# Optimization experiments

Hardware: AMD Instinct MI355X
Metric: run time of the kernel (lower is better)

Reference implementation:

```python
import jax, jax.numpy as jnp
import numpy as np

E, IN, OUT, GS, N = 8, 1024, 2816, 64, 2048
G = IN // GS  # 16 quantization groups along in_features


def setup_inputs() -> dict:
    key = jax.random.key(0)
    k0, k1, k2, k3 = jax.random.split(key, 4)
    x = jax.random.normal(k0, (N, IN), dtype=jnp.float32)
    # tokens are contiguous per expert; counts must sum exactly to N
    cuts = np.sort(np.random.default_rng(0).integers(0, N + 1, size=E - 1))
    counts = np.diff(np.concatenate([[0], cuts, [N]]))
    tokens_per_expert = jnp.asarray(counts, dtype=jnp.int32)
    # int4 codes stored as int32 in [0, 16)
    W_q = jax.random.randint(k1, (E, IN, OUT), 0, 16, dtype=jnp.int32)
    scales = jax.random.uniform(k2, (E, G, OUT), dtype=jnp.float32, minval=1e-3, maxval=2e-2)
    zeros = jax.random.uniform(k3, (E, G, OUT), dtype=jnp.float32, minval=0.0, maxval=15.0)
    return {"input": x, "tokens_per_expert": tokens_per_expert,
            "W_q": W_q, "scales": scales, "zeros": zeros}


def _dequant(W_q, scales, zeros):
    # HQQ-style asymmetric dequant: W = (W_q - zero) * scale, per group of GS
    # rows along in_features.  W_q: [E, IN, OUT] -> [E, G, GS, OUT]
    e, in_f, out_f = W_q.shape
    g = scales.shape[1]
    gs = in_f // g
    Wf = W_q.astype(scales.dtype).reshape(e, g, gs, out_f)
    W = (Wf - zeros[:, :, None, :]) * scales[:, :, None, :]
    return W.reshape(e, in_f, out_f)


def reference(input, tokens_per_expert, W_q, scales, zeros):
    # Dequantize all expert weights: [E, IN, OUT]
    W = _dequant(W_q, scales, zeros)
    # Expert id per token from exclusive-cumsum boundaries (tokens are sorted
    # by expert, contiguous slices [cumsum[e], cumsum[e+1]) ).
    boundaries = jnp.cumsum(tokens_per_expert)  # [E]
    tok = jnp.arange(input.shape[0])
    seg = jnp.searchsorted(boundaries, tok, side='right')  # [N] expert per token
    # Grouped GEMM expressed densely (jit-safe): compute x @ W_e for all e,
    # then select each token's own expert output.
    y_all = jnp.einsum('nd,edo->neo', input, W)  # [N, E, OUT]
    y = jnp.take_along_axis(y_all, seg[:, None, None], axis=1)[:, 0, :]
    return y
```

## Files before the change

### kernel.cpp

```cpp
#include <hip/hip_runtime.h>
#include <hip/hip_bf16.h>
#include <stdint.h>


namespace {
constexpr int kE = 8;
constexpr int kIn = 1024;
constexpr int kOut = 2816;
constexpr int kGroups = 16;
constexpr int kTok = 2048;
constexpr int kXStride = kIn + 64;
constexpr int kBM = 64;
constexpr int kBN = 128;
constexpr int kBTS = 72;
constexpr int kNT = kOut / kBN;
constexpr int kGrid = kNT * 256;
}

typedef __attribute__((ext_vector_type(8))) short short8;
typedef __attribute__((ext_vector_type(4))) float f32x4;
typedef __attribute__((ext_vector_type(4))) int i32x4;
typedef __attribute__((ext_vector_type(4))) unsigned int u32x4;

static __device__ __forceinline__ uint32_t fbits(float f) {
  union { float f; uint32_t u; } v; v.f = f; return v.u;
}
static __device__ __forceinline__ unsigned short bf16_rne(float f) {
  uint32_t u = fbits(f);
  u += 0x7fffu + ((u >> 16) & 1u);
  return (unsigned short)(u >> 16);
}
static __device__ __forceinline__ float bf16_f(unsigned short h) {
  union { uint32_t u; float f; } v; v.u = ((uint32_t)h) << 16; return v.f;
}

__global__ __launch_bounds__(256) void hqq_prep(const float* __restrict__ x,
                                                unsigned short* __restrict__ xhi,
                                                unsigned short* __restrict__ xlo) {
  const int row = blockIdx.x;
  const int tid = threadIdx.x;
  const f32x4 v = *(const f32x4*)(x + (size_t)row * kIn + tid * 4);
  unsigned long long hp = 0, lp = 0;
  float s = 0.f;
#pragma unroll
  for (int j = 0; j < 4; ++j) {
    float f = v[j];
    unsigned short h = bf16_rne(f);
    unsigned short l = bf16_rne(f - bf16_f(h));
    hp |= ((unsigned long long)h) << (16 * j);
    lp |= ((unsigned long long)l) << (16 * j);
    s += f;
  }
  *(unsigned long long*)(xhi + (size_t)row * kXStride + tid * 4) = hp;
  *(unsigned long long*)(xlo + (size_t)row * kXStride + tid * 4) = lp;
#pragma unroll
  for (int m = 1; m <= 8; m <<= 1) s += __shfl_xor(s, m, 64);
  if ((tid & 15) == 0) {
    const int g = tid >> 4;
    unsigned short rhi = bf16_rne(s);
    unsigned short rlo = bf16_rne(s - bf16_f(rhi));
    unsigned short* p = xhi + (size_t)row * kXStride + kIn;
    p[g] = rhi; p[16 + g] = rhi; p[32 + g] = rlo; p[48 + g] = 0;
    unsigned short* q = xlo + (size_t)row * kXStride + kIn;
    q[g] = 0; q[16 + g] = 0; q[32 + g] = 0; q[48 + g] = 0;
  }
}

__global__ __launch_bounds__(256, 2) void hqq_gemm(
    const unsigned short* __restrict__ xhi, const unsigned short* __restrict__ xlo,
    const int* __restrict__ wq, const float* __restrict__ scales,
    const float* __restrict__ zeros, const int* __restrict__ tpe,
    float* __restrict__ out) {
  __shared__ unsigned short Bt[2][kBN * kBTS];

  const int raw = blockIdx.x;
  const int bid = (raw & 7) * (kGrid / 8) + (raw >> 3);

  const int nt = bid >> 8;
  const int em = bid & 255;
  const int e = em >> 5;
  const int mt = em & 31;

  int e_start = 0, cnt = 0, cum = 0;
#pragma unroll
  for (int i = 0; i < kE; ++i) {
    int c = tpe[i];
    if (i == e) { e_start = cum; cnt = c; }
    cum += c;
  }
  if (mt * kBM >= cnt) return;
  const int e_end = e_start + cnt;
  const int row0 = e_start + mt * kBM;
  const int nn = nt * kBN;

  const int tid = threadIdx.x;
  const int lane = tid & 63;
  const int wid = tid >> 6;
  const int wm = wid >> 1;
  const int wn = wid & 1;

  size_t arow[2];
#pragma unroll
  for (int mf = 0; mf < 2; ++mf) {
    int r = row0 + wm * 32 + mf * 16 + (lane & 15);
    if (r > kTok - 1) r = kTok - 1;
    arow[mf] = (size_t)r * kXStride;
  }

  const int oq = tid & 31;
  const int kc = tid >> 5;
  const int* wbase = wq + (size_t)e * kIn * kOut + (size_t)(kc * 8) * kOut + nn + oq * 4;
  const int btw_off = (oq * 4) * kBTS + kc * 8;

  const float* sc_base = scales + (size_t)e * kGroups * kOut + nn + wn * 64 + (lane & 15);

  i32x4 w[8];
  auto loadB = [&](int g) {
    const int* p = wbase + (size_t)g * 64 * kOut;
#pragma unroll
    for (int i = 0; i < 8; ++i) w[i] = *(const i32x4*)(p + (size_t)i * kOut);
  };
  auto writeB = [&](int buf) {
    unsigned short* btw = &Bt[buf][btw_off];
#pragma unroll
    for (int j = 0; j < 4; ++j) {
      u32x4 o;
#pragma unroll
      for (int ww = 0; ww < 4; ++ww) {
        uint32_t b0 = fbits((float)w[2 * ww][j]);
        uint32_t b1 = fbits((float)w[2 * ww + 1][j]);
        o[ww] = (b0 >> 16) | (b1 & 0xffff0000u);
      }
      *(u32x4*)(btw + j * kBTS) = o;
    }
  };

  f32x4 acc[2][4];
#pragma unroll
  for (int a = 0; a < 2; ++a)
#pragma unroll
    for (int b = 0; b < 4; ++b) acc[a][b] = 0.f;

  loadB(0);
  writeB(0);
  __syncthreads();

  for (int g = 0; g <= 16; ++g) {
    if (g < 15) loadB(g + 1);

    float sc[4];
#pragma unroll
    for (int nf = 0; nf < 4; ++nf)
      sc[nf] = (g < kGroups) ? sc_base[(size_t)g * kOut + nf * 16] : 1.f;

    f32x4 S[2][4];
#pragma unroll
    for (int a = 0; a < 2; ++a)
#pragma unroll
      for (int b = 0; b < 4; ++b) S[a][b] = 0.f;

    const unsigned short* btb = &Bt[g & 1][0];
#pragma unroll
    for (int ks = 0; ks < 2; ++ks) {
      const int k0l = ks * 32 + (lane >> 4) * 8;
      const int k0g = g * 64 + k0l;
      short8 ah[2], al[2], bb[4];
#pragma unroll
      for (int mf = 0; mf < 2; ++mf) {
        ah[mf] = *(const short8*)&xhi[arow[mf] + k0g];
        al[mf] = *(const short8*)&xlo[arow[mf] + k0g];
      }
#pragma unroll
      for (int nf = 0; nf < 4; ++nf) {
        const int nrow = wn * 64 + nf * 16 + (lane & 15);
        bb[nf] = *(const short8*)&btb[nrow * kBTS + k0l];
      }
#pragma unroll
      for (int mf = 0; mf < 2; ++mf)
#pragma unroll
        for (int nf = 0; nf < 4; ++nf) {
          S[mf][nf] = __builtin_amdgcn_mfma_f32_16x16x32_bf16(ah[mf], bb[nf], S[mf][nf], 0, 0, 0);
          S[mf][nf] = __builtin_amdgcn_mfma_f32_16x16x32_bf16(al[mf], bb[nf], S[mf][nf], 0, 0, 0);
        }
    }
#pragma unroll
    for (int mf = 0; mf < 2; ++mf)
#pragma unroll
      for (int nf = 0; nf < 4; ++nf) acc[mf][nf] += sc[nf] * S[mf][nf];

    if (g < 15) {
      writeB((g + 1) & 1);
    } else if (g == 15) {
      const int o = tid >> 1;
      const int h = tid & 1;
      const float* zp = zeros + (size_t)e * kGroups * kOut + nn + o;
      const float* sp = scales + (size_t)e * kGroups * kOut + nn + o;
      unsigned short zh[16], zl[16];
#pragma unroll
      for (int gg = 0; gg < 16; ++gg) {
        float zsv = -(zp[(size_t)gg * kOut] * sp[(size_t)gg * kOut]);
        unsigned short hh = bf16_rne(zsv);
        zh[gg] = hh;
        zl[gg] = bf16_rne(zsv - bf16_f(hh));
      }
      unsigned short* wrow = &Bt[0][o * kBTS];
      auto pack8 = [](const unsigned short* u) {
        u32x4 r;
#pragma unroll
        for (int ww = 0; ww < 4; ++ww)
          r[ww] = (uint32_t)u[2 * ww] | ((uint32_t)u[2 * ww + 1] << 16);
        return r;
      };
      if (h == 0) {
        *(u32x4*)(wrow + 0)  = pack8(zh);
        *(u32x4*)(wrow + 8)  = pack8(zh + 8);
        *(u32x4*)(wrow + 16) = pack8(zl);
        *(u32x4*)(wrow + 24) = pack8(zl + 8);
      } else {
        *(u32x4*)(wrow + 32) = pack8(zh);
        *(u32x4*)(wrow + 40) = pack8(zh + 8);
        u32x4 z; z[0] = z[1] = z[2] = z[3] = 0;
        *(u32x4*)(wrow + 48) = z;
        *(u32x4*)(wrow + 56) = z;
      }
    }
    if (g < 16) __syncthreads();
  }

  float* ob = out + nn + wn * 64 + (lane & 15);
#pragma unroll
  for (int mf = 0; mf < 2; ++mf)
#pragma unroll
    for (int i = 0; i < 4; ++i) {
      const int t = row0 + wm * 32 + mf * 16 + (lane >> 4) * 4 + i;
      if (t < e_end) {
#pragma unroll
        for (int nf = 0; nf < 4; ++nf)
          ob[(size_t)t * kOut + nf * 16] = acc[mf][nf][i];
      }
    }
}

extern "C" void kernel_launch(void* const* d_in, const int* in_sizes, int n_in,
                              void* d_out, int out_size, void* d_ws, size_t ws_size,
                              hipStream_t stream) {
  const float* x = (const float*)d_in[0];
  const int* tpe = (const int*)d_in[1];
  const int* wq = (const int*)d_in[2];
  const float* scales = (const float*)d_in[3];
  const float* zeros = (const float*)d_in[4];
  float* out = (float*)d_out;

  unsigned short* xhi = (unsigned short*)d_ws;
  unsigned short* xlo = xhi + (size_t)kTok * kXStride;

  hqq_prep<<<dim3(kTok), dim3(256), 0, stream>>>(x, xhi, xlo);
  hqq_gemm<<<dim3(kGrid), dim3(256), 0, stream>>>(xhi, xlo, wq, scales, zeros, tpe, out);
}
```

Baseline: 266.5 us.

## Software-pipeline A/B loads two stages ahead with swizzled LDS and register ping-pong

```diff
diff --git a/kernel.cpp b/kernel.cpp
--- a/kernel.cpp
+++ b/kernel.cpp
@@ -22,6 +22,8 @@
 typedef __attribute__((ext_vector_type(4))) int i32x4;
 typedef __attribute__((ext_vector_type(4))) unsigned int u32x4;
 
+struct AFrag { short8 h0[2], l0[2], h1[2], l1[2]; };
+
 static __device__ __forceinline__ uint32_t fbits(float f) {
   union { float f; uint32_t u; } v; v.f = f; return v.u;
 }
@@ -32,6 +34,13 @@
 }
 static __device__ __forceinline__ float bf16_f(unsigned short h) {
   union { uint32_t u; float f; } v; v.u = ((uint32_t)h) << 16; return v.f;
+}
+static __device__ __forceinline__ u32x4 pack8(const unsigned short* u) {
+  u32x4 r;
+#pragma unroll
+  for (int ww = 0; ww < 4; ++ww)
+    r[ww] = (uint32_t)u[2 * ww] | ((uint32_t)u[2 * ww + 1] << 16);
+  return r;
 }
 
 __global__ __launch_bounds__(256) void hqq_prep(const float* __restrict__ x,
@@ -66,6 +75,144 @@
   }
 }
 
+
+#define ALOAD(g1, AF)                                                   \
+  {                                                                     \
+    _Pragma("unroll")                                                   \
+    for (int mf_ = 0; mf_ < 2; ++mf_) {                                 \
+      AF.h0[mf_] = *(const short8*)&xhi[arow[mf_] + (g1) * 64 + klane]; \
+      AF.l0[mf_] = *(const short8*)&xlo[arow[mf_] + (g1) * 64 + klane]; \
+      AF.h1[mf_] = *(const short8*)&xhi[arow[mf_] + (g1) * 64 + 32 + klane]; \
+      AF.l1[mf_] = *(const short8*)&xlo[arow[mf_] + (g1) * 64 + 32 + klane]; \
+    }                                                                   \
+  }
+
+#define LOADB(g, W)                                                     \
+  {                                                                     \
+    const int* p_ = wbase + (size_t)(g) * 64 * kOut;                    \
+    _Pragma("unroll")                                                   \
+    for (int i_ = 0; i_ < 8; ++i_) W[i_] = *(const i32x4*)(p_ + (size_t)i_ * kOut); \
+  }
+
+#define WRITEB(buf, W)                                                  \
+  {                                                                     \
+    unsigned short* btw_ = &Bt[buf][(oq * 4) * kBTS + (((kc + oq) & 7) * 8)]; \
+    _Pragma("unroll")                                                   \
+    for (int j_ = 0; j_ < 4; ++j_) {                                    \
+      u32x4 o_;                                                         \
+      _Pragma("unroll")                                                 \
+      for (int ww_ = 0; ww_ < 4; ++ww_) {                               \
+        uint32_t b0_ = fbits((float)W[2 * ww_][j_]);                    \
+        uint32_t b1_ = fbits((float)W[2 * ww_ + 1][j_]);                \
+        o_[ww_] = (b0_ >> 16) | (b1_ & 0xffff0000u);                    \
+      }                                                                 \
+      *(u32x4*)(btw_ + j_ * kBTS) = o_;                                 \
+    }                                                                   \
+  }
+
+#define ZSLOAD()                                                        \
+  {                                                                     \
+    _Pragma("unroll")                                                   \
+    for (int gg_ = 0; gg_ < 16; ++gg_) {                                \
+      zv[gg_] = zrow[(size_t)gg_ * kOut];                               \
+      sv[gg_] = srow[(size_t)gg_ * kOut];                               \
+    }                                                                   \
+  }
+
+#define PSEUDOWRITE()                                                   \
+  {                                                                     \
+    unsigned short zh_[16], zl_[16];                                    \
+    _Pragma("unroll")                                                   \
+    for (int gg_ = 0; gg_ < 16; ++gg_) {                                \
+      float zs_ = -(zv[gg_] * sv[gg_]);                                 \
+      unsigned short hh_ = bf16_rne(zs_);                               \
+      zh_[gg_] = hh_; zl_[gg_] = bf16_rne(zs_ - bf16_f(hh_));           \
+    }                                                                   \
+    unsigned short* wrow_ = &Bt[0][o_ps * kBTS];                        \
+    const int rq_ = (o_ps >> 2) & 7;                                    \
+    if (h_ps == 0) {                                                    \
+      *(u32x4*)(wrow_ + (((0 + rq_) & 7) * 8)) = pack8(zh_);            \
+      *(u32x4*)(wrow_ + (((1 + rq_) & 7) * 8)) = pack8(zh_ + 8);        \
+      *(u32x4*)(wrow_ + (((2 + rq_) & 7) * 8)) = pack8(zl_);            \
+      *(u32x4*)(wrow_ + (((3 + rq_) & 7) * 8)) = pack8(zl_ + 8);        \
+    } else {                                                            \
+      u32x4 zz_; zz_[0] = zz_[1] = zz_[2] = zz_[3] = 0;                 \
+      *(u32x4*)(wrow_ + (((4 + rq_) & 7) * 8)) = pack8(zh_);            \
+      *(u32x4*)(wrow_ + (((5 + rq_) & 7) * 8)) = pack8(zh_ + 8);        \
+      *(u32x4*)(wrow_ + (((6 + rq_) & 7) * 8)) = zz_;                   \
+      *(u32x4*)(wrow_ + (((7 + rq_) & 7) * 8)) = zz_;                   \
+    }                                                                   \
+  }
+
+#define MFMA_PHASE(g, AS)                                               \
+  {                                                                     \
+    f32x4 S[2][4];                                                      \
+    _Pragma("unroll")                                                   \
+    for (int a_ = 0; a_ < 2; ++a_)                                      \
+      _Pragma("unroll")                                                 \
+      for (int b_ = 0; b_ < 4; ++b_) S[a_][b_] = 0.f;                   \
+    const unsigned short* btb_ = &Bt[(g) & 1][0];                       \
+    {                                                                   \
+      short8 bb[4];                                                     \
+      _Pragma("unroll")                                                 \
+      for (int nf_ = 0; nf_ < 4; ++nf_)                                 \
+        bb[nf_] = *(const short8*)&btb_[broff0[nf_]];                   \
+      _Pragma("unroll")                                                 \
+      for (int mf_ = 0; mf_ < 2; ++mf_)                                 \
+        _Pragma("unroll")                                               \
+        for (int nf_ = 0; nf_ < 4; ++nf_) {                             \
+          S[mf_][nf_] = __builtin_amdgcn_mfma_f32_16x16x32_bf16(AS.h0[mf_], bb[nf_], S[mf_][nf_], 0, 0, 0); \
+          S[mf_][nf_] = __builtin_amdgcn_mfma_f32_16x16x32_bf16(AS.l0[mf_], bb[nf_], S[mf_][nf_], 0, 0, 0); \
+        }                                                               \
+    }                                                                   \
+    {                                                                   \
+      short8 bb[4];                                                     \
+      _Pragma("unroll")                                                 \
+      for (int nf_ = 0; nf_ < 4; ++nf_)                                 \
+        bb[nf_] = *(const short8*)&btb_[broff1[nf_]];                   \
+      _Pragma("unroll")                                                 \
+      for (int mf_ = 0; mf_ < 2; ++mf_)                                 \
+        _Pragma("unroll")                                               \
+        for (int nf_ = 0; nf_ < 4; ++nf_) {                             \
+          S[mf_][nf_] = __builtin_amdgcn_mfma_f32_16x16x32_bf16(AS.h1[mf_], bb[nf_], S[mf_][nf_], 0, 0, 0); \
+          S[mf_][nf_] = __builtin_amdgcn_mfma_f32_16x16x32_bf16(AS.l1[mf_], bb[nf_], S[mf_][nf_], 0, 0, 0); \
+        }                                                               \
+    }                                                                   \
+    _Pragma("unroll")                                                   \
+    for (int mf_ = 0; mf_ < 2; ++mf_)                                   \
+      _Pragma("unroll")                                                 \
+      for (int nf_ = 0; nf_ < 4; ++nf_) acc[mf_][nf_] += sc_cur[nf_] * S[mf_][nf_]; \
+  }
+
+#define BODY(g, AFILL, ASPEND, WFILL, WSPEND)                           \
+  {                                                                     \
+    ALOAD((g) + 1, AFILL);                                              \
+    __builtin_amdgcn_sched_barrier(0);                                  \
+    if ((g) <= 13) {                                                    \
+      LOADB((g) + 2, WFILL);                                            \
+    } else if ((g) == 14) {                                             \
+      ZSLOAD();                                                         \
+    }                                                                   \
+    if ((g) <= 14) {                                                    \
+      _Pragma("unroll")                                                 \
+      for (int nf_ = 0; nf_ < 4; ++nf_)                                 \
+        sc_nxt[nf_] = sc_base[(size_t)((g) + 1) * kOut + nf_ * 16];     \
+    } else {                                                            \
+      _Pragma("unroll")                                                 \
+      for (int nf_ = 0; nf_ < 4; ++nf_) sc_nxt[nf_] = 1.f;              \
+    }                                                                   \
+    __builtin_amdgcn_sched_barrier(0);                                  \
+    MFMA_PHASE(g, ASPEND);                                              \
+    _Pragma("unroll")                                                   \
+    for (int nf_ = 0; nf_ < 4; ++nf_) sc_cur[nf_] = sc_nxt[nf_];        \
+    if ((g) <= 14) {                                                    \
+      WRITEB(((g) + 1) & 1, WSPEND);                                    \
+    } else {                                                            \
+      PSEUDOWRITE();                                                    \
+    }                                                                   \
+    asm volatile("s_waitcnt lgkmcnt(0)\n\ts_barrier" ::: "memory");     \
+  }
+
 __global__ __launch_bounds__(256, 2) void hqq_gemm(
     const unsigned short* __restrict__ xhi, const unsigned short* __restrict__ xlo,
     const int* __restrict__ wq, const float* __restrict__ scales,
@@ -106,126 +253,52 @@
     if (r > kTok - 1) r = kTok - 1;
     arow[mf] = (size_t)r * kXStride;
   }
+  const int klane = (lane >> 4) * 8;
+
+  int broff0[4], broff1[4];
+#pragma unroll
+  for (int nf = 0; nf < 4; ++nf) {
+    const int nrow = wn * 64 + nf * 16 + (lane & 15);
+    const int gk = lane >> 4;
+    broff0[nf] = nrow * kBTS + (((gk + (nrow >> 2)) & 7) * 8);
+    broff1[nf] = nrow * kBTS + (((gk + 4 + (nrow >> 2)) & 7) * 8);
+  }
 
   const int oq = tid & 31;
   const int kc = tid >> 5;
   const int* wbase = wq + (size_t)e * kIn * kOut + (size_t)(kc * 8) * kOut + nn + oq * 4;
-  const int btw_off = (oq * 4) * kBTS + kc * 8;
 
   const float* sc_base = scales + (size_t)e * kGroups * kOut + nn + wn * 64 + (lane & 15);
 
-  i32x4 w[8];
-  auto loadB = [&](int g) {
-    const int* p = wbase + (size_t)g * 64 * kOut;
-#pragma unroll
-    for (int i = 0; i < 8; ++i) w[i] = *(const i32x4*)(p + (size_t)i * kOut);
-  };
-  auto writeB = [&](int buf) {
-    unsigned short* btw = &Bt[buf][btw_off];
-#pragma unroll
-    for (int j = 0; j < 4; ++j) {
-      u32x4 o;
-#pragma unroll
-      for (int ww = 0; ww < 4; ++ww) {
-        uint32_t b0 = fbits((float)w[2 * ww][j]);
-        uint32_t b1 = fbits((float)w[2 * ww + 1][j]);
-        o[ww] = (b0 >> 16) | (b1 & 0xffff0000u);
-      }
-      *(u32x4*)(btw + j * kBTS) = o;
-    }
-  };
-
+  const int o_ps = tid >> 1;
+  const int h_ps = tid & 1;
+  const float* zrow = zeros + (size_t)e * kGroups * kOut + nn + o_ps;
+  const float* srow = scales + (size_t)e * kGroups * kOut + nn + o_ps;
+
+  i32x4 wA[8], wB[8];
+  AFrag aA, aB;
+  float zv[16], sv[16];
+  float sc_cur[4], sc_nxt[4];
   f32x4 acc[2][4];
 #pragma unroll
   for (int a = 0; a < 2; ++a)
 #pragma unroll
     for (int b = 0; b < 4; ++b) acc[a][b] = 0.f;
 
-  loadB(0);
-  writeB(0);
-  __syncthreads();
-
-  for (int g = 0; g <= 16; ++g) {
-    if (g < 15) loadB(g + 1);
-
-    float sc[4];
-#pragma unroll
-    for (int nf = 0; nf < 4; ++nf)
-      sc[nf] = (g < kGroups) ? sc_base[(size_t)g * kOut + nf * 16] : 1.f;
-
-    f32x4 S[2][4];
-#pragma unroll
-    for (int a = 0; a < 2; ++a)
-#pragma unroll
-      for (int b = 0; b < 4; ++b) S[a][b] = 0.f;
-
-    const unsigned short* btb = &Bt[g & 1][0];
-#pragma unroll
-    for (int ks = 0; ks < 2; ++ks) {
-      const int k0l = ks * 32 + (lane >> 4) * 8;
-      const int k0g = g * 64 + k0l;
-      short8 ah[2], al[2], bb[4];
-#pragma unroll
-      for (int mf = 0; mf < 2; ++mf) {
-        ah[mf] = *(const short8*)&xhi[arow[mf] + k0g];
-        al[mf] = *(const short8*)&xlo[arow[mf] + k0g];
-      }
-#pragma unroll
-      for (int nf = 0; nf < 4; ++nf) {
-        const int nrow = wn * 64 + nf * 16 + (lane & 15);
-        bb[nf] = *(const short8*)&btb[nrow * kBTS + k0l];
-      }
-#pragma unroll
-      for (int mf = 0; mf < 2; ++mf)
-#pragma unroll
-        for (int nf = 0; nf < 4; ++nf) {
-          S[mf][nf] = __builtin_amdgcn_mfma_f32_16x16x32_bf16(ah[mf], bb[nf], S[mf][nf], 0, 0, 0);
-          S[mf][nf] = __builtin_amdgcn_mfma_f32_16x16x32_bf16(al[mf], bb[nf], S[mf][nf], 0, 0, 0);
-        }
-    }
-#pragma unroll
-    for (int mf = 0; mf < 2; ++mf)
-#pragma unroll
-      for (int nf = 0; nf < 4; ++nf) acc[mf][nf] += sc[nf] * S[mf][nf];
-
-    if (g < 15) {
-      writeB((g + 1) & 1);
-    } else if (g == 15) {
-      const int o = tid >> 1;
-      const int h = tid & 1;
-      const float* zp = zeros + (size_t)e * kGroups * kOut + nn + o;
-      const float* sp = scales + (size_t)e * kGroups * kOut + nn + o;
-      unsigned short zh[16], zl[16];
-#pragma unroll
-      for (int gg = 0; gg < 16; ++gg) {
-        float zsv = -(zp[(size_t)gg * kOut] * sp[(size_t)gg * kOut]);
-        unsigned short hh = bf16_rne(zsv);
-        zh[gg] = hh;
-        zl[gg] = bf16_rne(zsv - bf16_f(hh));
-      }
-      unsigned short* wrow = &Bt[0][o * kBTS];
-      auto pack8 = [](const unsigned short* u) {
-        u32x4 r;
-#pragma unroll
-        for (int ww = 0; ww < 4; ++ww)
-          r[ww] = (uint32_t)u[2 * ww] | ((uint32_t)u[2 * ww + 1] << 16);
-        return r;
-      };
-      if (h == 0) {
-        *(u32x4*)(wrow + 0)  = pack8(zh);
-        *(u32x4*)(wrow + 8)  = pack8(zh + 8);
-        *(u32x4*)(wrow + 16) = pack8(zl);
-        *(u32x4*)(wrow + 24) = pack8(zl + 8);
-      } else {
-        *(u32x4*)(wrow + 32) = pack8(zh);
-        *(u32x4*)(wrow + 40) = pack8(zh + 8);
-        u32x4 z; z[0] = z[1] = z[2] = z[3] = 0;
-        *(u32x4*)(wrow + 48) = z;
-        *(u32x4*)(wrow + 56) = z;
-      }
-    }
-    if (g < 16) __syncthreads();
-  }
+  LOADB(0, wB);
+  WRITEB(0, wB);
+  LOADB(1, wB);
+  ALOAD(0, aA);
+#pragma unroll
+  for (int nf = 0; nf < 4; ++nf) sc_cur[nf] = sc_base[nf * 16];
+  asm volatile("s_waitcnt lgkmcnt(0)\n\ts_barrier" ::: "memory");
+
+  for (int gg = 0; gg < 16; gg += 2) {
+    BODY(gg, aB, aA, wA, wB);
+    BODY(gg + 1, aA, aB, wB, wA);
+  }
+
+  MFMA_PHASE(0, aA);
 
   float* ob = out + nn + wn * 64 + (lane & 15);
 #pragma unroll
```

Result: slower. 494.1 us (+85.4%).
